# Kernel tuning notes

Hardware: AMD Instinct MI355X
Metric: run time of the kernel (lower is better)

Reference implementation:

```python
import jax, jax.numpy as jnp
import numpy as np

N = 128          # number of nodes (particles)
NR = N * (N - 1) # number of directed edges, receiver-major order
B = 128          # batch
C = 16           # channel dim


def setup_inputs() -> dict:
    key = jax.random.key(0)
    x = jax.random.normal(key, (B, NR, C), dtype=jnp.float32)
    # assign_matrices enumerates (r, s) pairs receiver-major, so edge i has
    # receiver i // (N-1); Rr2 is the one-hot indicator of this mapping.
    receivers = jnp.arange(NR, dtype=jnp.int32) // (N - 1)
    return {"x": x, "receivers": receivers}


def reference(x, receivers):
    # exp of edge scores
    e = jnp.exp(x)  # [B, Nr, C]
    # tensordot(exp, Rr2, axes=[1,1]) == segment-sum over edges grouped by receiver
    seg = jax.ops.segment_sum(e.transpose(1, 0, 2), receivers, num_segments=N)  # [N, B, C]
    # tensordot(exp_sum, Rr2, axes=1) == gather each edge's receiver sum back to edges
    denom = seg[receivers]                 # [Nr, B, C]
    denom = denom.transpose(1, 2, 0)       # [B, C, Nr]
    # NOTE: the original divides the raw inputs (not exp) by the summed exp
    return x.transpose(0, 2, 1) / denom    # [B, C, Nr]
```

## Files before the change

### kernel.cpp

```cpp
#include <hip/hip_runtime.h>

#define NN   128
#define NE   127
#define CH   16
#define NRE  (NN * NE)
#define STR  128

__global__ __launch_bounds__(256) void attn2_kernel(const float* __restrict__ x,
                                                    float* __restrict__ out) {
    __shared__ float tile[4][CH * STR];

    const int t   = threadIdx.x & 63;
    const int w   = threadIdx.x >> 6;
    const int seg = (blockIdx.x << 2) | w;
    const int b   = seg >> 7;
    const int r   = seg & (NN - 1);

    float* T = tile[w];

    const float4* xseg = (const float4*)(x + (size_t)seg * NE * CH);

    float4 v[8];
    #pragma unroll
    for (int it = 0; it < 8; ++it) {
        int f = t + (it << 6);
        v[it] = xseg[f < 508 ? f : 507];
    }

    const int p  = (t & 3) << 2;
    const int er = t >> 2;
    float a0 = 0.f, a1 = 0.f, a2 = 0.f, a3 = 0.f;
    #pragma unroll
    for (int it = 0; it < 8; ++it) {
        int f = t + (it << 6);
        if (f < 508) {
            int edge = er + (it << 4);
            T[(p + 0) * STR + edge] = v[it].x;
            T[(p + 1) * STR + edge] = v[it].y;
            T[(p + 2) * STR + edge] = v[it].z;
            T[(p + 3) * STR + edge] = v[it].w;
            a0 += __expf(v[it].x); a1 += __expf(v[it].y);
            a2 += __expf(v[it].z); a3 += __expf(v[it].w);
        }
    }

    #pragma unroll
    for (int m = 4; m <= 32; m <<= 1) {
        a0 += __shfl_xor(a0, m, 64);
        a1 += __shfl_xor(a1, m, 64);
        a2 += __shfl_xor(a2, m, 64);
        a3 += __shfl_xor(a3, m, 64);
    }
    if (t < 4) {
        T[(p + 0) * STR + NE] = 1.0f / a0;
        T[(p + 1) * STR + NE] = 1.0f / a1;
        T[(p + 2) * STR + NE] = 1.0f / a2;
        T[(p + 3) * STR + NE] = 1.0f / a3;
    }
    __syncthreads();

    float* oseg = out + (size_t)b * CH * NRE + (size_t)r * NE;
    #pragma unroll
    for (int c = 0; c < CH; ++c) {
        float rd = T[c * STR + NE];
        float* row = oseg + (size_t)c * NRE;
        row[t] = T[c * STR + t] * rd;
        if (t < 63) row[64 + t] = T[c * STR + 64 + t] * rd;
    }
}

extern "C" void kernel_launch(void* const* d_in, const int* in_sizes, int n_in,
                              void* d_out, int out_size, void* d_ws, size_t ws_size,
                              hipStream_t stream) {
    const float* x = (const float*)d_in[0];
    float* out = (float*)d_out;
    attn2_kernel<<<(128 * 128) / 4, 256, 0, stream>>>(x, out);
}
```

Before: 234.7 us.

## Transpose each segment through LDS in two 64-edge halves with padded stride

Each wave's LDS tile shrinks to a 66-float row stride and is filled in two 64-edge halves, each written out before the next is staged. This halves the LDS footprint and breaks the stride-128 pattern that sends every channel row to the same bank. The per-channel reciprocal sums are now broadcast from registers with a wave shuffle, so the LDS slot for them and the __syncthreads go away. Dropping the barrier relies on each wave using only its own tile and on LDS accesses staying in order within a wave.

New measurement: 258.6 us. 10.2% more time.

```diff
diff --git a/kernel.cpp b/kernel.cpp
--- a/kernel.cpp
+++ b/kernel.cpp
@@ -4,7 +4,7 @@
 #define NE   127
 #define CH   16
 #define NRE  (NN * NE)
-#define STR  128
+#define STR  66
 
 __global__ __launch_bounds__(256) void attn2_kernel(const float* __restrict__ x,
                                                     float* __restrict__ out) {
@@ -15,35 +15,30 @@
     const int seg = (blockIdx.x << 2) | w;
     const int b   = seg >> 7;
     const int r   = seg & (NN - 1);
-
     float* T = tile[w];
 
     const float4* xseg = (const float4*)(x + (size_t)seg * NE * CH);
 
     float4 v[8];
     #pragma unroll
-    for (int it = 0; it < 8; ++it) {
-        int f = t + (it << 6);
-        v[it] = xseg[f < 508 ? f : 507];
+    for (int k = 0; k < 8; ++k) {
+        int f = t + (k << 6);
+        v[k] = xseg[f < 508 ? f : 507];
     }
 
-    const int p  = (t & 3) << 2;
+    const int g  = t & 3;
+    const int p  = g << 2;
     const int er = t >> 2;
+
     float a0 = 0.f, a1 = 0.f, a2 = 0.f, a3 = 0.f;
     #pragma unroll
-    for (int it = 0; it < 8; ++it) {
-        int f = t + (it << 6);
+    for (int k = 0; k < 8; ++k) {
+        int f = t + (k << 6);
         if (f < 508) {
-            int edge = er + (it << 4);
-            T[(p + 0) * STR + edge] = v[it].x;
-            T[(p + 1) * STR + edge] = v[it].y;
-            T[(p + 2) * STR + edge] = v[it].z;
-            T[(p + 3) * STR + edge] = v[it].w;
-            a0 += __expf(v[it].x); a1 += __expf(v[it].y);
-            a2 += __expf(v[it].z); a3 += __expf(v[it].w);
+            a0 += __expf(v[k].x); a1 += __expf(v[k].y);
+            a2 += __expf(v[k].z); a3 += __expf(v[k].w);
         }
     }
-
     #pragma unroll
     for (int m = 4; m <= 32; m <<= 1) {
         a0 += __shfl_xor(a0, m, 64);
@@ -51,21 +46,42 @@
         a2 += __shfl_xor(a2, m, 64);
         a3 += __shfl_xor(a3, m, 64);
     }
-    if (t < 4) {
-        T[(p + 0) * STR + NE] = 1.0f / a0;
-        T[(p + 1) * STR + NE] = 1.0f / a1;
-        T[(p + 2) * STR + NE] = 1.0f / a2;
-        T[(p + 3) * STR + NE] = 1.0f / a3;
-    }
-    __syncthreads();
+    const float r0 = 1.0f / a0, r1 = 1.0f / a1, r2 = 1.0f / a2, r3 = 1.0f / a3;
 
     float* oseg = out + (size_t)b * CH * NRE + (size_t)r * NE;
+
+    #pragma unroll
+    for (int k = 0; k < 4; ++k) {
+        int e = er + (k << 4);
+        T[(p + 0) * STR + e] = v[k].x;
+        T[(p + 1) * STR + e] = v[k].y;
+        T[(p + 2) * STR + e] = v[k].z;
+        T[(p + 3) * STR + e] = v[k].w;
+    }
     #pragma unroll
     for (int c = 0; c < CH; ++c) {
-        float rd = T[c * STR + NE];
-        float* row = oseg + (size_t)c * NRE;
-        row[t] = T[c * STR + t] * rd;
-        if (t < 63) row[64 + t] = T[c * STR + 64 + t] * rd;
+        float rg = (c & 3) == 0 ? r0 : (c & 3) == 1 ? r1 : (c & 3) == 2 ? r2 : r3;
+        float rd = __shfl(rg, c >> 2, 64);
+        oseg[(size_t)c * NRE + t] = T[c * STR + t] * rd;
+    }
+
+    #pragma unroll
+    for (int k = 4; k < 8; ++k) {
+        int f = t + (k << 6);
+        if (f < 508) {
+            int e = er + (k << 4) - 64;
+            T[(p + 0) * STR + e] = v[k].x;
+            T[(p + 1) * STR + e] = v[k].y;
+            T[(p + 2) * STR + e] = v[k].z;
+            T[(p + 3) * STR + e] = v[k].w;
+        }
+    }
+    #pragma unroll
+    for (int c = 0; c < CH; ++c) {
+        float rg = (c & 3) == 0 ? r0 : (c & 3) == 1 ? r1 : (c & 3) == 2 ? r2 : r3;
+        float rd = __shfl(rg, c >> 2, 64);
+        if (t < 63)
+            oseg[(size_t)c * NRE + 64 + t] = T[c * STR + t] * rd;
     }
 }
 
```
